# Optimization experiments

Hardware: AMD Instinct MI355X
Metric: run time of the kernel (lower is better)

Reference implementation:

```python
import jax, jax.numpy as jnp
import numpy as np


def _positional_embedding(C, M, dtype):
    # pe[pos, 0::2] = sin(pos*div), pe[pos, 1::2] = cos(pos*div)
    pos = jnp.arange(M, dtype=jnp.float32)[:, None]                      # [M,1]
    div = jnp.exp(jnp.arange(0, C, 2, dtype=jnp.float32) * (-np.log(10000.0) / C))  # [C/2]
    ang = pos * div                                                      # [M,C/2]
    pe = jnp.stack([jnp.sin(ang), jnp.cos(ang)], axis=-1).reshape(M, C)  # interleave
    return pe.T.astype(dtype)                                            # [C,M]


def setup_inputs() -> dict:
    key = jax.random.key(0)
    k1, k2, k3 = jax.random.split(key, 3)
    B, C, M, K = 64, 512, 1024, 5
    h_in = jax.random.normal(k1, (B, C, 1, M), dtype=jnp.float32)
    conv_w = jax.random.normal(k2, (C, K), dtype=jnp.float32) * 0.1
    conv_b = jax.random.normal(k3, (C,), dtype=jnp.float32) * 0.1
    return {"h_in": h_in, "conv_w": conv_w, "conv_b": conv_b}


def reference(h_in, conv_w, conv_b):
    B, C, _, M = h_in.shape
    K = conv_w.shape[1]
    p = (K - 1) // 2
    dt = h_in.dtype

    hb = h_in                                              # pre-PE copy
    pe = _positional_embedding(C, M, dt)                   # [C,M]
    x = h_in + pe[None, :, None, :]                        # [B,C,1,M]

    # adaptive avg pool to 1 over (H,W)
    y = jnp.mean(x, axis=(2, 3))                           # [B,C]
    # unfold along channel axis with padding p, window K
    y_pad = jnp.pad(y, ((0, 0), (p, p)))                   # [B,C+2p]
    idx = jnp.arange(C)[:, None] + jnp.arange(K)[None, :]  # [C,K]
    y_unf = y_pad[:, idx]                                  # [B,C,K]
    # grouped conv1d -> per-channel dot over window, then sigmoid gate
    gate = jax.nn.sigmoid(jnp.einsum('bck,ck->bc', y_unf, conv_w) + conv_b)  # [B,C]

    h = x * gate[:, :, None, None]                         # dropout = identity (eval)

    hs = h[:, :, 0, :]                                     # [B,C,M]
    hbs = hb[:, :, 0, :]                                   # [B,C,M]
    I_hat = (jnp.eye(M, dtype=dt) / M) - (1.0 / (M * M))   # [M,M] centering matrix

    t1 = jnp.einsum('bcm,mn->bcn', hs, I_hat)
    t2 = jnp.einsum('bcm,mn->bcn', hbs, I_hat)
    cov = (jnp.einsum('bcn,bdn->bcd', t1, hs)
           + jnp.einsum('bcn,bdn->bcd', t2, hbs)
           + jnp.eye(C, dtype=dt) * 1e-8)                  # [B,C,C]
    return cov
```

## Files before the change

### kernel.cpp

```cpp
#include <hip/hip_runtime.h>
#include <math.h>

#define B_N 64
#define C_N 512
#define M_N 1024
#define K_W 2048

typedef __attribute__((ext_vector_type(8))) short bf16x8;
typedef __attribute__((ext_vector_type(4))) float f32x4;

__device__ __forceinline__ unsigned short f2b(float f) {
  unsigned int x = __builtin_bit_cast(unsigned int, f);
  unsigned int lsb = (x >> 16) & 1u;
  x += 0x7fffu + lsb;
  return (unsigned short)(x >> 16);
}

typedef __attribute__((address_space(1))) const unsigned int gas_uint;
typedef __attribute__((address_space(3))) unsigned int las_uint;
__device__ __forceinline__ void async_ld(const void* g, const void* l) {
  __builtin_amdgcn_global_load_lds((gas_uint*)(uintptr_t)g,
                                   (las_uint*)(unsigned int)(uintptr_t)l, 16, 0, 0);
}

__global__ void k_pe(float* __restrict__ pe, float* __restrict__ pesum) {
  int c = blockIdx.x, m = threadIdx.x;
  float freq = expf((float)(c & ~1) * (-9.210340371976184f / 512.0f));
  float ang = (float)m * freq;
  float v = (c & 1) ? cosf(ang) : sinf(ang);
  pe[c * M_N + m] = v;
  float s = v;
  for (int off = 32; off; off >>= 1) s += __shfl_down(s, off);
  __shared__ float ws[16];
  if ((m & 63) == 0) ws[m >> 6] = s;
  __syncthreads();
  if (m < 16) {
    float t = ws[m];
    for (int off = 8; off; off >>= 1) t += __shfl_down(t, off);
    if (m == 0) pesum[c] = t;
  }
}

__global__ void k_rs(const float* __restrict__ src, float* __restrict__ rb) {
  size_t e = ((size_t)blockIdx.x * 256 + threadIdx.x) * 8;
  const float4* s4 = (const float4*)(src + e);
  float4 v0 = s4[0], v1 = s4[1];
  float s = v0.x + v0.y + v0.z + v0.w + v1.x + v1.y + v1.z + v1.w;
  for (int off = 32; off; off >>= 1) s += __shfl_down(s, off);
  if ((threadIdx.x & 63) == 0) atomicAdd(&rb[e >> 10], s);
}

__global__ void k_gate(const float* __restrict__ wp, const float* __restrict__ bp,
                       const float* __restrict__ rb0, const float* __restrict__ pesum,
                       float* __restrict__ u, float* __restrict__ rbF,
                       float* __restrict__ gateF) {
  int idx = blockIdx.x * 256 + threadIdx.x;
  int b = idx >> 9, c = idx & (C_N - 1);
  float rbv = rb0[idx];
  float rx = rbv + pesum[c];
  float acc = 0.f;
  for (int k = 0; k < 5; ++k) {
    int cc = c + k - 2;
    if (cc < 0 || cc >= C_N) continue;
    float y = (rb0[b * C_N + cc] + pesum[cc]) * (1.0f / 1024.0f);
    acc += y * wp[c * 5 + k];
  }
  float g = 1.0f / (1.0f + expf(-(acc + bp[c])));
  gateF[idx] = g;
  u[idx] = g * rx;
  rbF[idx] = rbv;
}

__global__ void k_x(float* __restrict__ hbase, const float* __restrict__ pe,
                    const float* __restrict__ gateF) {
  int row = blockIdx.x;
  int c = row & (C_N - 1), t = threadIdx.x;
  float* rp = hbase + (size_t)row * M_N;
  float4 h4 = ((const float4*)rp)[t];
  float4 p4 = ((const float4*)(pe + (size_t)c * M_N))[t];
  float g = gateF[row];
  union { uint2 v; unsigned short us[4]; } H, X;
  H.us[0] = f2b(h4.x); H.us[1] = f2b(h4.y); H.us[2] = f2b(h4.z); H.us[3] = f2b(h4.w);
  X.us[0] = f2b(g * (h4.x + p4.x)); X.us[1] = f2b(g * (h4.y + p4.y));
  X.us[2] = f2b(g * (h4.z + p4.z)); X.us[3] = f2b(g * (h4.w + p4.w));
  __syncthreads();
  unsigned short* wr = (unsigned short*)rp;
  ((uint2*)wr)[t] = H.v;
  ((uint2*)(wr + M_N))[t] = X.v;
}

__device__ __forceinline__ void cov_stage(unsigned short (*tl)[128 * 32],
                                          const unsigned short* srcp, int wsel,
                                          int ldst) {
  for (int g = 0; g < 4; g++)
    async_ld(srcp + (size_t)g * (16 * K_W), &tl[wsel][ldst + g * 512]);
}

template <int VM, bool STG>
__device__ __forceinline__ void cov_step(
    unsigned short (*tiles)[2][128 * 32], int it, const unsigned short* srcp,
    int wsel, int ldst, int wr, int wc, int fr, int fcol, f32x4 (&acc)[4][4]) {
  asm volatile("s_waitcnt vmcnt(%0)" ::"n"(VM) : "memory");
  __builtin_amdgcn_sched_barrier(0);
  __builtin_amdgcn_s_barrier();
  __builtin_amdgcn_sched_barrier(0);
  int cur = it & 3;
  bf16x8 bf[4], af[4];
  for (int j = 0; j < 4; j++)
    bf[j] = *(const bf16x8*)&tiles[cur][1][(wc + j * 16 + fr) * 32 + fcol];
  for (int i = 0; i < 4; i++)
    af[i] = *(const bf16x8*)&tiles[cur][0][(wr + i * 16 + fr) * 32 + fcol];
  if (STG) cov_stage(tiles[(it + 3) & 3], srcp + (size_t)(it + 3) * 32, wsel, ldst);
  asm volatile("s_waitcnt lgkmcnt(0)" ::: "memory");
  __builtin_amdgcn_sched_barrier(0);
  __builtin_amdgcn_s_setprio(1);
  for (int i = 0; i < 4; i++)
    for (int j = 0; j < 4; j++)
      acc[i][j] = __builtin_amdgcn_mfma_f32_16x16x32_bf16(af[i], bf[j], acc[i][j], 0, 0, 0);
  __builtin_amdgcn_s_setprio(0);
}

__global__ __launch_bounds__(256, 2)
void k_cov(const unsigned short* __restrict__ W, const float* __restrict__ aux,
           float* __restrict__ out, int b0) {
  __shared__ unsigned short tiles[4][2][128 * 32];
  int t = threadIdx.x, lane = t & 63, w = t >> 6;
  int bid = blockIdx.x;
  int xcd = bid & 7, i5 = bid >> 3;
  int b = b0 + xcd * 4 + (i5 >> 4);
  int s = i5 & 15;
  int cblk = (s >> 2) * 128, dblk = (s & 3) * 128;

  int rowbase = (w & 1) ? dblk : cblk;
  int half = w >> 1, wsel = w & 1;
  int gcol = (lane & 3) ^ ((lane >> 3) & 3);
  const unsigned short* srcp = W + (size_t)b * (C_N * K_W)
      + (size_t)(rowbase + half * 64 + (lane >> 2)) * K_W + gcol * 8;
  int ldst = half * 2048;

  int wr = (w >> 1) * 64, wc = (w & 1) * 64;
  int fr = lane & 15, kc = lane >> 4;
  int fcol = (kc ^ ((fr >> 1) & 3)) * 8;

  f32x4 acc[4][4];
  const f32x4 z = {0.f, 0.f, 0.f, 0.f};
  for (int i = 0; i < 4; i++) for (int j = 0; j < 4; j++) acc[i][j] = z;

  for (int s0 = 0; s0 < 3; ++s0)
    cov_stage(tiles[s0], srcp + (size_t)s0 * 32, wsel, ldst);

  for (int it = 0; it < 61; ++it)
    cov_step<8, true>(tiles, it, srcp, wsel, ldst, wr, wc, fr, fcol, acc);
  cov_step<8, false>(tiles, 61, srcp, wsel, ldst, wr, wc, fr, fcol, acc);
  cov_step<4, false>(tiles, 62, srcp, wsel, ldst, wr, wc, fr, fcol, acc);
  cov_step<0, false>(tiles, 63, srcp, wsel, ldst, wr, wc, fr, fcol, acc);

  const float invM = 1.0f / 1024.0f, invM2 = invM * invM;
  const float* ub = aux + (size_t)b * C_N;
  const float* rbb = aux + (size_t)B_N * C_N + (size_t)b * C_N;
  for (int i = 0; i < 4; i++)
    for (int r = 0; r < 4; r++) {
      int c = cblk + wr + i * 16 + kc * 4 + r;
      float uc = ub[c], rbc = rbb[c];
      for (int j = 0; j < 4; j++) {
        int d = dblk + wc + j * 16 + fr;
        float v = acc[i][j][r] * invM - (uc * ub[d] + rbc * rbb[d]) * invM2;
        if (c == d) v += 1e-8f;
        out[((size_t)b * C_N + c) * C_N + d] = v;
      }
    }
}

extern "C" void kernel_launch(void* const* d_in, const int* in_sizes, int n_in,
                              void* d_out, int out_size, void* d_ws, size_t ws_size,
                              hipStream_t stream) {
  const float* h32 = (const float*)d_in[0];
  const float* conv_w = (const float*)d_in[1];
  const float* conv_b = (const float*)d_in[2];
  char* OUT = (char*)d_out;
  char* HIN = (char*)d_in[0];

  char* AUXA = OUT + (48ull << 20);
  float* uA    = (float*)(AUXA);
  float* rbA   = (float*)(AUXA + (128 << 10));
  float* gateF = (float*)(AUXA + (256 << 10));
  float* rb0   = (float*)(AUXA + (384 << 10));
  float* pesum = (float*)(AUXA + (512 << 10));
  float* peF   = (float*)(OUT + (49ull << 20));
  char* AUXB = HIN;

  hipMemsetAsync(rb0, 0, 128 << 10, stream);
  k_pe<<<C_N, 1024, 0, stream>>>(peF, pesum);
  k_rs<<<16384, 256, 0, stream>>>(h32, rb0);
  k_gate<<<(B_N * C_N) / 256, 256, 0, stream>>>(conv_w, conv_b, rb0, pesum,
                                                uA, rbA, gateF);
  k_x<<<B_N * C_N, 256, 0, stream>>>((float*)HIN, peF, gateF);

  k_cov<<<512, 256, 0, stream>>>((const unsigned short*)HIN, uA, (float*)d_out, 0);
  hipMemcpyAsync(AUXB, AUXA, 256 << 10, hipMemcpyDeviceToDevice, stream);
  k_cov<<<512, 256, 0, stream>>>((const unsigned short*)HIN, (const float*)AUXB,
                                 (float*)d_out, 32);
}
```

Measured before the change: 329.3 us.

## Exploit covariance symmetry: compute upper-triangle tiles and mirror-write transposes

The covariance kernel now computes only the 10 upper-triangular 128x128 tiles per batch and writes each off-diagonal tile a second time, transposed through LDS, which roughly halves the MFMA work and operand loads. The LDS pipeline drops from 4 to 3 stages so three blocks can fit per CU, and stage indices become compile-time constants. The row-sum kernel replaces per-wave atomics with a block-level reduction and plain stores, which also removes the memset. When a workspace is available the aux data goes there, so a single 640-block launch replaces two launches with a copy in between, at the cost of extra transpose writes and a shallower prefetch.

```diff
diff --git a/kernel.cpp b/kernel.cpp
--- a/kernel.cpp
+++ b/kernel.cpp
@@ -42,12 +42,17 @@
 }
 
 __global__ void k_rs(const float* __restrict__ src, float* __restrict__ rb) {
-  size_t e = ((size_t)blockIdx.x * 256 + threadIdx.x) * 8;
+  __shared__ float ws[4];
+  int t = threadIdx.x;
+  size_t e = ((size_t)blockIdx.x * 256 + t) * 8;
   const float4* s4 = (const float4*)(src + e);
   float4 v0 = s4[0], v1 = s4[1];
   float s = v0.x + v0.y + v0.z + v0.w + v1.x + v1.y + v1.z + v1.w;
   for (int off = 32; off; off >>= 1) s += __shfl_down(s, off);
-  if ((threadIdx.x & 63) == 0) atomicAdd(&rb[e >> 10], s);
+  if ((t & 63) == 0) ws[t >> 6] = s;
+  __syncthreads();
+  if (t == 0) rb[blockIdx.x * 2] = ws[0] + ws[1];
+  if (t == 128) rb[blockIdx.x * 2 + 1] = ws[2] + ws[3];
 }
 
 __global__ void k_gate(const float* __restrict__ wp, const float* __restrict__ bp,
@@ -96,7 +101,7 @@
     async_ld(srcp + (size_t)g * (16 * K_W), &tl[wsel][ldst + g * 512]);
 }
 
-template <int VM, bool STG>
+template <int VM, bool STG, int CUR>
 __device__ __forceinline__ void cov_step(
     unsigned short (*tiles)[2][128 * 32], int it, const unsigned short* srcp,
     int wsel, int ldst, int wr, int wc, int fr, int fcol, f32x4 (&acc)[4][4]) {
@@ -104,13 +109,13 @@
   __builtin_amdgcn_sched_barrier(0);
   __builtin_amdgcn_s_barrier();
   __builtin_amdgcn_sched_barrier(0);
-  int cur = it & 3;
   bf16x8 bf[4], af[4];
   for (int j = 0; j < 4; j++)
-    bf[j] = *(const bf16x8*)&tiles[cur][1][(wc + j * 16 + fr) * 32 + fcol];
+    bf[j] = *(const bf16x8*)&tiles[CUR][1][(wc + j * 16 + fr) * 32 + fcol];
   for (int i = 0; i < 4; i++)
-    af[i] = *(const bf16x8*)&tiles[cur][0][(wr + i * 16 + fr) * 32 + fcol];
-  if (STG) cov_stage(tiles[(it + 3) & 3], srcp + (size_t)(it + 3) * 32, wsel, ldst);
+    af[i] = *(const bf16x8*)&tiles[CUR][0][(wr + i * 16 + fr) * 32 + fcol];
+  if (STG)
+    cov_stage(tiles[(CUR + 2) % 3], srcp + (size_t)(it + 2) * 32, wsel, ldst);
   asm volatile("s_waitcnt lgkmcnt(0)" ::: "memory");
   __builtin_amdgcn_sched_barrier(0);
   __builtin_amdgcn_s_setprio(1);
@@ -120,16 +125,18 @@
   __builtin_amdgcn_s_setprio(0);
 }
 
-__global__ __launch_bounds__(256, 2)
+__global__ __launch_bounds__(256, 3)
 void k_cov(const unsigned short* __restrict__ W, const float* __restrict__ aux,
-           float* __restrict__ out, int b0) {
-  __shared__ unsigned short tiles[4][2][128 * 32];
+           float* __restrict__ out, int b0, int bpx) {
+  __shared__ unsigned short tiles[3][2][128 * 32];
   int t = threadIdx.x, lane = t & 63, w = t >> 6;
   int bid = blockIdx.x;
   int xcd = bid & 7, i5 = bid >> 3;
-  int b = b0 + xcd * 4 + (i5 >> 4);
-  int s = i5 & 15;
-  int cblk = (s >> 2) * 128, dblk = (s & 3) * 128;
+  int b = b0 + xcd * bpx + i5 / 10;
+  int s = i5 % 10;
+  int ti = (s >= 1) + (s >= 3) + (s >= 6);
+  int tj = s - ti * (ti + 1) / 2;
+  int cblk = ti * 128, dblk = tj * 128;
 
   int rowbase = (w & 1) ? dblk : cblk;
   int half = w >> 1, wsel = w & 1;
@@ -146,14 +153,18 @@
   const f32x4 z = {0.f, 0.f, 0.f, 0.f};
   for (int i = 0; i < 4; i++) for (int j = 0; j < 4; j++) acc[i][j] = z;
 
-  for (int s0 = 0; s0 < 3; ++s0)
-    cov_stage(tiles[s0], srcp + (size_t)s0 * 32, wsel, ldst);
-
-  for (int it = 0; it < 61; ++it)
-    cov_step<8, true>(tiles, it, srcp, wsel, ldst, wr, wc, fr, fcol, acc);
-  cov_step<8, false>(tiles, 61, srcp, wsel, ldst, wr, wc, fr, fcol, acc);
-  cov_step<4, false>(tiles, 62, srcp, wsel, ldst, wr, wc, fr, fcol, acc);
-  cov_step<0, false>(tiles, 63, srcp, wsel, ldst, wr, wc, fr, fcol, acc);
+  cov_stage(tiles[0], srcp, wsel, ldst);
+  cov_stage(tiles[1], srcp + 32, wsel, ldst);
+
+  for (int it = 0; it < 60; it += 3) {
+    cov_step<4, true, 0>(tiles, it + 0, srcp, wsel, ldst, wr, wc, fr, fcol, acc);
+    cov_step<4, true, 1>(tiles, it + 1, srcp, wsel, ldst, wr, wc, fr, fcol, acc);
+    cov_step<4, true, 2>(tiles, it + 2, srcp, wsel, ldst, wr, wc, fr, fcol, acc);
+  }
+  cov_step<4, true, 0>(tiles, 60, srcp, wsel, ldst, wr, wc, fr, fcol, acc);
+  cov_step<4, true, 1>(tiles, 61, srcp, wsel, ldst, wr, wc, fr, fcol, acc);
+  cov_step<4, false, 2>(tiles, 62, srcp, wsel, ldst, wr, wc, fr, fcol, acc);
+  cov_step<0, false, 0>(tiles, 63, srcp, wsel, ldst, wr, wc, fr, fcol, acc);
 
   const float invM = 1.0f / 1024.0f, invM2 = invM * invM;
   const float* ub = aux + (size_t)b * C_N;
@@ -169,6 +180,37 @@
         out[((size_t)b * C_N + c) * C_N + d] = v;
       }
     }
+
+  if (ti != tj) {
+    float* tb = (float*)tiles;
+    for (int hp = 0; hp < 2; ++hp) {
+      __syncthreads();
+      if ((w >> 1) == hp) {
+        for (int i = 0; i < 4; i++)
+          for (int j = 0; j < 4; j++)
+            for (int r = 0; r < 4; r++) {
+              int ch = i * 16 + kc * 4 + r;
+              int dl = wc + j * 16 + fr;
+              tb[ch * 128 + (dl ^ (ch & 31))] = acc[i][j][r];
+            }
+      }
+      __syncthreads();
+      for (int p = 0; p < 8; ++p) {
+        int dl = p * 16 + (t >> 4);
+        int cl = (t & 15) * 4;
+        int dg = dblk + dl;
+        float ud = ub[dg], rbd = rbb[dg];
+        float4 o;
+        float* op = (float*)&o;
+        for (int q = 0; q < 4; ++q) {
+          int cg = cblk + hp * 64 + cl + q;
+          float raw = tb[(cl + q) * 128 + (dl ^ ((cl + q) & 31))];
+          op[q] = raw * invM - (ub[cg] * ud + rbb[cg] * rbd) * invM2;
+        }
+        *(float4*)&out[((size_t)b * C_N + dg) * C_N + (cblk + hp * 64 + cl)] = o;
+      }
+    }
+  }
 }
 
 extern "C" void kernel_launch(void* const* d_in, const int* in_sizes, int n_in,
@@ -180,24 +222,29 @@
   char* OUT = (char*)d_out;
   char* HIN = (char*)d_in[0];
 
-  char* AUXA = OUT + (48ull << 20);
-  float* uA    = (float*)(AUXA);
-  float* rbA   = (float*)(AUXA + (128 << 10));
-  float* gateF = (float*)(AUXA + (256 << 10));
-  float* rb0   = (float*)(AUXA + (384 << 10));
-  float* pesum = (float*)(AUXA + (512 << 10));
+  char* SCR = OUT + (48ull << 20);
+  float* rb0   = (float*)SCR;
+  float* pesum = (float*)(SCR + (128 << 10));
+  float* gateF = (float*)(SCR + (192 << 10));
   float* peF   = (float*)(OUT + (49ull << 20));
-  char* AUXB = HIN;
-
-  hipMemsetAsync(rb0, 0, 128 << 10, stream);
+
+  bool ws_ok = (d_ws != nullptr) && (ws_size >= (size_t)(256 << 10));
+  float* uX = ws_ok ? (float*)d_ws : (float*)(SCR + (512 << 10));
+
   k_pe<<<C_N, 1024, 0, stream>>>(peF, pesum);
   k_rs<<<16384, 256, 0, stream>>>(h32, rb0);
   k_gate<<<(B_N * C_N) / 256, 256, 0, stream>>>(conv_w, conv_b, rb0, pesum,
-                                                uA, rbA, gateF);
+                                                uX, uX + B_N * C_N, gateF);
   k_x<<<B_N * C_N, 256, 0, stream>>>((float*)HIN, peF, gateF);
 
-  k_cov<<<512, 256, 0, stream>>>((const unsigned short*)HIN, uA, (float*)d_out, 0);
-  hipMemcpyAsync(AUXB, AUXA, 256 << 10, hipMemcpyDeviceToDevice, stream);
-  k_cov<<<512, 256, 0, stream>>>((const unsigned short*)HIN, (const float*)AUXB,
-                                 (float*)d_out, 32);
-}
+  if (ws_ok) {
+    k_cov<<<640, 256, 0, stream>>>((const unsigned short*)HIN, uX,
+                                   (float*)d_out, 0, 8);
+  } else {
+    k_cov<<<320, 256, 0, stream>>>((const unsigned short*)HIN, uX,
+                                   (float*)d_out, 0, 4);
+    hipMemcpyAsync(HIN, uX, 256 << 10, hipMemcpyDeviceToDevice, stream);
+    k_cov<<<320, 256, 0, stream>>>((const unsigned short*)HIN, (const float*)HIN,
+                                   (float*)d_out, 32, 4);
+  }
+}
```

Result: faster. 300.3 us (-8.8%).
